# Kernel tuning notes

Measured on AMD Instinct MI355X. Metric: run time of the kernel, lower is better.

The kernel has to match this reference:

```python
import jax, jax.numpy as jnp
import numpy as np

LAMBDA_A = 1.0
NUM_ITER = 3
K = 64
BN_EPS = 1e-5


def setup_inputs() -> dict:
    key = jax.random.key(0)
    ks = jax.random.split(key, 8)
    B, C, H, W = 16, 512, 64, 64
    x = jax.random.normal(ks[0], (B, C, H, W), dtype=jnp.float32)
    # codebook mu: init normal(std~sqrt(2/k)) then L2-normalize along dim=1 (k axis), as in torch init
    mu = jax.random.normal(ks[1], (C, K), dtype=jnp.float32) * np.sqrt(2.0 / K)
    mu = mu / jnp.maximum(jnp.linalg.norm(mu, axis=1, keepdims=True), 1e-12)
    # 1x1 convs expressed as (out, in) matrices
    stem_w = jax.random.normal(ks[2], (C, C), dtype=jnp.float32) * np.sqrt(2.0 / C)
    stem_b = jnp.zeros((C,), dtype=jnp.float32)
    head_w = jax.random.normal(ks[3], (C, C), dtype=jnp.float32) * np.sqrt(2.0 / C)
    head_b = jnp.zeros((C,), dtype=jnp.float32)
    bn_gamma = jnp.ones((C,), dtype=jnp.float32)
    bn_beta = jnp.zeros((C,), dtype=jnp.float32)
    return {"x": x, "mu": mu, "stem_w": stem_w, "stem_b": stem_b,
            "head_w": head_w, "head_b": head_b,
            "bn_gamma": bn_gamma, "bn_beta": bn_beta}


def _conv1x1(x, w, b):
    # x: (B,C,H,W), w: (O,C)
    return jnp.einsum('bchw,oc->bohw', x, w) + b[None, :, None, None]


def reference(x, mu, stem_w, stem_b, head_w, head_b, bn_gamma, bn_beta):
    B, C, H, W = x.shape
    N = H * W
    y = _conv1x1(x, stem_w, stem_b)                 # (B,C,H,W)
    yf = y.reshape(B, C, N).transpose(0, 2, 1)      # (B,N,C)

    mu_b = jnp.broadcast_to(mu[None], (B, C, K))    # (B,C,K)
    z = None
    for _ in range(NUM_ITER):
        z = jax.nn.softmax(LAMBDA_A * jnp.einsum('bnc,bck->bnk', yf, mu_b), axis=2)
        zn = z / (1e-6 + z.sum(axis=1, keepdims=True))
        mu_b = jnp.einsum('bnc,bnk->bck', yf, zn)
        mu_b = mu_b / jnp.maximum(jnp.linalg.norm(mu_b, axis=1, keepdims=True), 1e-12)

    # EM loop runs under no_grad in torch
    mu_b = jax.lax.stop_gradient(mu_b)
    z = jax.lax.stop_gradient(z)

    y2 = jnp.einsum('bck,bnk->bcn', mu_b, z).reshape(B, C, H, W)

    # head: ReLU -> 1x1 conv -> BatchNorm2d (training-mode batch stats)
    h = _conv1x1(jnp.maximum(y2, 0.0), head_w, head_b)
    mean = h.mean(axis=(0, 2, 3), keepdims=True)
    var = h.var(axis=(0, 2, 3), keepdims=True)
    h = (h - mean) * jax.lax.rsqrt(var + BN_EPS)
    h = h * bn_gamma[None, :, None, None] + bn_beta[None, :, None, None]

    return jnp.maximum(h + x, 0.0)
```

## Files before the change

### kernel.cpp

```cpp
#include <hip/hip_runtime.h>


typedef _Float16 half_t;
typedef _Float16 half4 __attribute__((ext_vector_type(4)));
typedef _Float16 half8 __attribute__((ext_vector_type(8)));
typedef float f32x4 __attribute__((ext_vector_type(4)));

#define GLD_LDS(gp, lp) __builtin_amdgcn_global_load_lds( \
    (const __attribute__((address_space(1))) void*)(gp),  \
    (__attribute__((address_space(3))) void*)(lp), 16, 0, 0)

#define SBAR __builtin_amdgcn_sched_barrier(0)
#define RAWBAR do { SBAR; __builtin_amdgcn_s_barrier(); SBAR; } while (0)

template <int L> __device__ __forceinline__ void vmwait() {
  if constexpr (L == 8) asm volatile("s_waitcnt vmcnt(8)" ::: "memory");
  else if constexpr (L == 6) asm volatile("s_waitcnt vmcnt(6)" ::: "memory");
  else asm volatile("s_waitcnt vmcnt(0)" ::: "memory");
}

constexpr int CB = 16;
constexpr int CC = 512;
constexpr int CN = 4096;
constexpr int CKK = 64;
constexpr long MALL = (long)CB * CN;

__device__ inline int swz8(int bid, int n) {
  return (bid & 7) * (n >> 3) + (bid >> 3);
}

__global__ __launch_bounds__(256) void prep(
    const float* __restrict__ stem_w, const float* __restrict__ head_w,
    const float* __restrict__ mu,
    half_t* __restrict__ swh, half_t* __restrict__ hwh,
    half_t* __restrict__ muT, half_t* __restrict__ muck)
{
  int i = blockIdx.x * 256 + threadIdx.x;
  swh[i] = (half_t)stem_w[i];
  hwh[i] = (half_t)head_w[i];
  if (i < CC * CKK) {
    int c = i >> 6, k = i & 63;
    half_t v = (half_t)mu[i];
    for (int b = 0; b < CB; ++b) {
      muT[(long)b * CKK * CC + (long)k * CC + c] = v;
      muck[(long)b * CC * CKK + i] = v;
    }
  }
}

__global__ __launch_bounds__(256) void xpose(
    const float* __restrict__ in, half_t* __restrict__ outT)
{
  __shared__ half_t t[64][65];
  const int s0 = blockIdx.x * 64, r0 = blockIdx.y * 64;
  const long bz = blockIdx.z;
  const float* ib = in + bz * (long)CC * CN;
  half_t* ob = outT + bz * (long)CC * CN;
  const int tid = threadIdx.x, cl = tid & 63, rw = tid >> 6;
#pragma unroll
  for (int it = 0; it < 16; ++it) {
    int r = it * 4 + rw;
    t[cl][r] = (half_t)ib[(long)(r0 + r) * CN + s0 + cl];
  }
  __syncthreads();
#pragma unroll
  for (int it = 0; it < 16; ++it) {
    int s = it * 4 + rw;
    ob[(long)(s0 + s) * CC + r0 + cl] = t[s][cl];
  }
}

template <int BM, int BN, int MODE, int EPI, bool SWZ>
__global__ __launch_bounds__(256) void gemm_abt(
    const half_t* __restrict__ A, const half_t* __restrict__ Bm,
    half_t* __restrict__ Co, half_t* __restrict__ CoT,
    float* __restrict__ Cacc, const float* __restrict__ bias,
    int M, int Nn, int Kk, int ksplit, long sA, long sB, long sC)
{
  constexpr int FM = BM / 32, FN = BN / 32;
  constexpr int HB = (BM + BN) * 64;
  constexpr int LCNT = (BM / 8) / 4 + (BN / 8) / 4;
  constexpr int STG = 2 * HB;
  constexpr int EPS = (EPI != 0) ? BN * (BM + 4) : 0;
  constexpr int TOT = STG > EPS ? STG : EPS;
  __shared__ __align__(16) half_t smem[TOT];

  const int tid = threadIdx.x, wid = tid >> 6, lane = tid & 63;
  int bid = blockIdx.x;
  if constexpr (SWZ) bid = swz8(bid, gridDim.x);
  const int tilesN = Nn / BN;
  const int tm = bid / tilesN, tn = bid % tilesN;
  const long bz = blockIdx.z;
  const half_t* Ab = A + bz * sA + (long)tm * BM * Kk;
  const half_t* Bb = Bm + bz * sB + (long)tn * BN * Kk;
  const int ksteps = Kk >> 6;
  const int per = ksteps / ksplit;
  const int ks0 = blockIdx.y * per, ks1 = ks0 + per;
  const int wr = wid >> 1, wc = wid & 1;

  const int r8 = lane >> 3;
  const int gcs = ((lane & 7) ^ r8) * 8;

  auto stage = [&](int ks, int buf) {
    half_t* dA = smem + buf * HB;
    half_t* dB = dA + BM * 64;
    const half_t* ga = Ab + (long)ks * 64;
#pragma unroll
    for (int c = wid; c < BM / 8; c += 4)
      GLD_LDS(ga + (long)(c * 8 + r8) * Kk + gcs, &dA[c * 512]);
    const half_t* gb = Bb + (long)ks * 64;
#pragma unroll
    for (int c = wid; c < BN / 8; c += 4)
      GLD_LDS(gb + (long)(c * 8 + r8) * Kk + gcs, &dB[c * 512]);
  };

  f32x4 acc[FM][FN];
#pragma unroll
  for (int i = 0; i < FM; ++i)
#pragma unroll
    for (int j = 0; j < FN; ++j) acc[i][j] = f32x4{0.f, 0.f, 0.f, 0.f};

  stage(ks0, 0);
  if (ks0 + 1 < ks1) { stage(ks0 + 1, 1); vmwait<LCNT>(); }
  else               { vmwait<0>(); }
  RAWBAR;

  int cur = 0;
  for (int ks = ks0; ks < ks1; ++ks) {
    const half_t* lA = smem + cur * HB;
    const half_t* lB = lA + BM * 64;
#pragma unroll
    for (int kk = 0; kk < 2; ++kk) {
      half8 af[FM], bfr[FN];
      const int cg = kk * 4 + (lane >> 4);
#pragma unroll
      for (int i = 0; i < FM; ++i) {
        const int rA = wr * (BM / 2) + i * 16 + (lane & 15);
        af[i] = *(const half8*)&lA[rA * 64 + ((cg ^ (rA & 7)) << 3)];
      }
#pragma unroll
      for (int j = 0; j < FN; ++j) {
        const int rB = wc * (BN / 2) + j * 16 + (lane & 15);
        bfr[j] = *(const half8*)&lB[rB * 64 + ((cg ^ (rB & 7)) << 3)];
      }
      __builtin_amdgcn_s_setprio(1);
#pragma unroll
      for (int i = 0; i < FM; ++i)
#pragma unroll
        for (int j = 0; j < FN; ++j)
          acc[i][j] = __builtin_amdgcn_mfma_f32_16x16x32_f16(af[i], bfr[j],
                                                             acc[i][j], 0, 0, 0);
      __builtin_amdgcn_s_setprio(0);
    }
    RAWBAR;
    const bool more = (ks + 2 < ks1);
    if (more) { stage(ks + 2, cur); vmwait<LCNT>(); }
    else      { vmwait<0>(); }
    RAWBAR;
    cur ^= 1;
  }

  if constexpr (EPI != 0) {
    static_assert(BM == 128 && BN == 128, "LDS epilogue assumes 128x128");
    constexpr int PIT = BM + 4;
    half_t* ep = smem;
#pragma unroll
    for (int j = 0; j < FN; ++j) {
      const int nl = wc * 64 + j * 16 + (lane & 15);
      float bv = 0.f;
      if constexpr (MODE & 1) bv = bias[tn * BN + nl];
#pragma unroll
      for (int i = 0; i < FM; ++i) {
        const int ml = wr * 64 + i * 16 + ((lane >> 4) << 2);
        half4 h;
#pragma unroll
        for (int r = 0; r < 4; ++r) {
          float v = acc[i][j][r] + bv;
          if constexpr (MODE & 2) v = fmaxf(v, 0.f);
          h[r] = (half_t)v;
        }
        *(half4*)&ep[nl * PIT + ml] = h;
      }
    }
    __syncthreads();
    const long rowbase = (long)tm * BM;
    if constexpr (EPI & 1) {
#pragma unroll
      for (int s = 0; s < 8; ++s) {
        const int q = tid + 256 * s;
        const int m = q & 127, cc = q >> 7;
        half8 v;
#pragma unroll
        for (int e = 0; e < 8; ++e) v[e] = ep[(cc * 8 + e) * PIT + m];
        *(half8*)&Co[bz * sC + (rowbase + m) * Nn + tn * BN + cc * 8] = v;
      }
    }
    if constexpr (EPI & 2) {
      const long b = rowbase >> 12, nbase = rowbase & 4095;
#pragma unroll
      for (int s = 0; s < 8; ++s) {
        const int q = tid + 256 * s;
        const int mc = q & 15;
        const int cl = q >> 4;
        half8 v = *(const half8*)&ep[cl * PIT + mc * 8];
        *(half8*)&CoT[(b * Nn + tn * BN + cl) * 4096 + nbase + mc * 8] = v;
      }
    }
  } else {
#pragma unroll
    for (int j = 0; j < FN; ++j) {
      const int n = tn * BN + wc * (BN / 2) + j * 16 + (lane & 15);
      float bv = 0.f;
      if constexpr (MODE & 1) bv = bias[n];
#pragma unroll
      for (int i = 0; i < FM; ++i) {
        const int mbase = tm * BM + wr * (BM / 2) + i * 16 + ((lane >> 4) << 2);
#pragma unroll
        for (int r = 0; r < 4; ++r) {
          const long idx = bz * sC + (long)(mbase + r) * Nn + n;
          if constexpr ((MODE & 4) != 0) {
            atomicAdd(&Cacc[idx], acc[i][j][r]);
          } else {
            float v = acc[i][j][r] + bv;
            if constexpr ((MODE & 2) != 0) v = fmaxf(v, 0.f);
            Co[idx] = (half_t)v;
          }
        }
      }
    }
  }
}

__global__ __launch_bounds__(256) void s_softmax(
    const half_t* __restrict__ Yf, const half_t* __restrict__ muT,
    half_t* __restrict__ zp, half_t* __restrict__ zT)
{
  constexpr int HB = (128 + 64) * 64;
  __shared__ __align__(16) union {
    half_t st[2 * HB];
    half_t zh[128 * 68];
  } sm;
  const int tid = threadIdx.x, wid = tid >> 6, lane = tid & 63;
  const int tm = blockIdx.x;
  const long bz = blockIdx.z;
  const half_t* Ab = Yf + bz * (long)CN * CC + (long)tm * 128 * CC;
  const half_t* Bb = muT + bz * (long)CKK * CC;

  const int r8 = lane >> 3;
  const int gcs = ((lane & 7) ^ r8) * 8;

  auto stage = [&](int ks, int buf) {
    half_t* dA = sm.st + buf * HB;
    half_t* dB = dA + 128 * 64;
    const half_t* ga = Ab + (long)ks * 64;
#pragma unroll
    for (int c = wid; c < 16; c += 4)
      GLD_LDS(ga + (long)(c * 8 + r8) * CC + gcs, &dA[c * 512]);
    const half_t* gb = Bb + (long)ks * 64;
#pragma unroll
    for (int c = wid; c < 8; c += 4)
      GLD_LDS(gb + (long)(c * 8 + r8) * CC + gcs, &dB[c * 512]);
  };

  f32x4 acc[2][4];
#pragma unroll
  for (int i = 0; i < 2; ++i)
#pragma unroll
    for (int j = 0; j < 4; ++j) acc[i][j] = f32x4{0.f, 0.f, 0.f, 0.f};

  stage(0, 0);
  stage(1, 1);
  vmwait<6>();
  RAWBAR;
  int cur = 0;
  for (int ks = 0; ks < 8; ++ks) {
    const half_t* lA = sm.st + cur * HB;
    const half_t* lB = lA + 128 * 64;
#pragma unroll
    for (int kk = 0; kk < 2; ++kk) {
      half8 af[2], bfr[4];
      const int cg = kk * 4 + (lane >> 4);
#pragma unroll
      for (int i = 0; i < 2; ++i) {
        const int rA = wid * 32 + i * 16 + (lane & 15);
        af[i] = *(const half8*)&lA[rA * 64 + ((cg ^ (rA & 7)) << 3)];
      }
#pragma unroll
      for (int j = 0; j < 4; ++j) {
        const int rB = j * 16 + (lane & 15);
        bfr[j] = *(const half8*)&lB[rB * 64 + ((cg ^ (rB & 7)) << 3)];
      }
      __builtin_amdgcn_s_setprio(1);
#pragma unroll
      for (int i = 0; i < 2; ++i)
#pragma unroll
        for (int j = 0; j < 4; ++j)
          acc[i][j] = __builtin_amdgcn_mfma_f32_16x16x32_f16(af[i], bfr[j],
                                                             acc[i][j], 0, 0, 0);
      __builtin_amdgcn_s_setprio(0);
    }
    RAWBAR;
    const bool more = (ks + 2 < 8);
    if (more) { stage(ks + 2, cur); vmwait<6>(); }
    else      { vmwait<0>(); }
    RAWBAR;
    cur ^= 1;
  }

#pragma unroll
  for (int i = 0; i < 2; ++i)
#pragma unroll
    for (int r = 0; r < 4; ++r) {
      float mx = fmaxf(fmaxf(acc[i][0][r], acc[i][1][r]),
                       fmaxf(acc[i][2][r], acc[i][3][r]));
#pragma unroll
      for (int m = 1; m < 16; m <<= 1) mx = fmaxf(mx, __shfl_xor(mx, m));
      float p[4], s = 0.f;
#pragma unroll
      for (int j = 0; j < 4; ++j) { p[j] = __expf(acc[i][j][r] - mx); s += p[j]; }
#pragma unroll
      for (int m = 1; m < 16; m <<= 1) s += __shfl_xor(s, m);
      const float inv = 1.f / s;
#pragma unroll
      for (int j = 0; j < 4; ++j) acc[i][j][r] = p[j] * inv;
    }

#pragma unroll
  for (int i = 0; i < 2; ++i)
#pragma unroll
    for (int j = 0; j < 4; ++j)
#pragma unroll
      for (int r = 0; r < 4; ++r) {
        const int row = wid * 32 + i * 16 + ((lane >> 4) << 2) + r;
        const int col = j * 16 + (lane & 15);
        sm.zh[row * 68 + col] = (half_t)acc[i][j][r];
      }
  __syncthreads();
  if (zp) {
    const int nl = tid >> 1, seg = tid & 1;
    const long base = bz * (long)CN * CKK + (long)(tm * 128 + nl) * CKK + seg * 32;
#pragma unroll
    for (int g = 0; g < 4; ++g) {
      half8 v;
#pragma unroll
      for (int e = 0; e < 8; ++e) v[e] = sm.zh[nl * 68 + seg * 32 + g * 8 + e];
      *(half8*)&zp[base + g * 8] = v;
    }
  }
  {
    const int k = tid >> 2, seg = tid & 3;
    const long base = bz * (long)CKK * CN + (long)k * CN + tm * 128 + seg * 32;
#pragma unroll
    for (int g = 0; g < 4; ++g) {
      half8 v;
#pragma unroll
      for (int e = 0; e < 8; ++e) v[e] = sm.zh[(seg * 32 + g * 8 + e) * 68 + k];
      *(half8*)&zT[base + g * 8] = v;
    }
  }
}

__global__ __launch_bounds__(64) void mu_norm(
    const float* __restrict__ acc, half_t* __restrict__ muT, half_t* __restrict__ muck)
{
  const int bk = blockIdx.x;
  const int b = bk >> 6, k = bk & 63;
  const float* row = acc + (long)bk * CC;
  const int t = threadIdx.x;
  float v[8]; float s = 0.f;
#pragma unroll
  for (int e = 0; e < 8; ++e) { v[e] = row[t * 8 + e]; s += v[e] * v[e]; }
#pragma unroll
  for (int m = 1; m < 64; m <<= 1) s += __shfl_xor(s, m);
  const float inv = 1.f / fmaxf(sqrtf(s), 1e-12f);
  half8 o;
#pragma unroll
  for (int e = 0; e < 8; ++e) o[e] = (half_t)(v[e] * inv);
  *(half8*)&muT[(long)bk * CC + t * 8] = o;
  half_t* mc = muck + (long)b * CC * CKK;
#pragma unroll
  for (int e = 0; e < 8; ++e) mc[(long)(t * 8 + e) * CKK + k] = o[e];
}

__global__ __launch_bounds__(256) void bn_stats2(
    const half_t* __restrict__ hcn, float* __restrict__ stats)
{
  const int c = blockIdx.x, tid = threadIdx.x;
  float s = 0.f, s2 = 0.f;
  for (int b = 0; b < CB; ++b) {
    const half_t* p = hcn + ((long)b * CC + c) * CN;
    for (int i = tid * 8; i < CN; i += 2048) {
      half8 v = *(const half8*)&p[i];
#pragma unroll
      for (int e = 0; e < 8; ++e) { float f = (float)v[e]; s += f; s2 += f * f; }
    }
  }
#pragma unroll
  for (int m = 1; m < 64; m <<= 1) { s += __shfl_xor(s, m); s2 += __shfl_xor(s2, m); }
  __shared__ float r[8];
  const int wid = tid >> 6;
  if ((tid & 63) == 0) { r[wid] = s; r[4 + wid] = s2; }
  __syncthreads();
  if (tid == 0) {
    stats[c] = r[0] + r[1] + r[2] + r[3];
    stats[CC + c] = r[4] + r[5] + r[6] + r[7];
  }
}

__global__ void bn_param(const float* __restrict__ stats,
                         const float* __restrict__ gamma, const float* __restrict__ beta,
                         float* __restrict__ scsh)
{
  const int c = threadIdx.x;
  const float cnt = 1.f / 65536.f;
  const float mean = stats[c] * cnt;
  const float var = stats[CC + c] * cnt - mean * mean;
  const float sc = gamma[c] * rsqrtf(var + 1e-5f);
  scsh[c] = sc;
  scsh[CC + c] = beta[c] - mean * sc;
}

__global__ __launch_bounds__(256) void bn_final2(
    const half_t* __restrict__ hcn, const float* __restrict__ x,
    const float* __restrict__ scsh, float* __restrict__ out)
{
  const long i8 = (long)blockIdx.x * 256 + threadIdx.x;
  const int c = (int)((i8 >> 9) & 511);
  const float sc = scsh[c], sh = scsh[CC + c];
  half8 h = *(const half8*)&hcn[i8 * 8];
  f32x4 x0 = *(const f32x4*)&x[i8 * 8];
  f32x4 x1 = *(const f32x4*)&x[i8 * 8 + 4];
  f32x4 o0, o1;
#pragma unroll
  for (int e = 0; e < 4; ++e) o0[e] = fmaxf((float)h[e] * sc + sh + x0[e], 0.f);
#pragma unroll
  for (int e = 0; e < 4; ++e) o1[e] = fmaxf((float)h[4 + e] * sc + sh + x1[e], 0.f);
  *(f32x4*)&out[i8 * 8] = o0;
  *(f32x4*)&out[i8 * 8 + 4] = o1;
}

extern "C" void kernel_launch(void* const* d_in, const int* in_sizes, int n_in,
                              void* d_out, int out_size, void* d_ws, size_t ws_size,
                              hipStream_t stream)
{
  const float* x      = (const float*)d_in[0];
  const float* mu     = (const float*)d_in[1];
  const float* stem_w = (const float*)d_in[2];
  const float* stem_b = (const float*)d_in[3];
  const float* head_w = (const float*)d_in[4];
  const float* head_b = (const float*)d_in[5];
  const float* bn_g   = (const float*)d_in[6];
  const float* bn_b   = (const float*)d_in[7];
  float* out = (float*)d_out;

  const size_t NEED = 214ull << 20;
  if (ws_size < NEED) {
    hipMemsetAsync(d_out, 0, (size_t)out_size * 4, stream);
    return;
  }
  char* ws = (char*)d_ws;
  const long MB = 1 << 20;
  half_t* xT   = (half_t*)(ws);
  half_t* Yf   = (half_t*)(ws + 64 * MB);
  half_t* ycn  = (half_t*)(ws + 128 * MB);
  half_t* z    = (half_t*)(ws + 192 * MB);
  half_t* zT   = (half_t*)(ws + 200 * MB);
  half_t* muT  = (half_t*)(ws + 208 * MB);
  half_t* muck = (half_t*)(ws + 209 * MB);
  float* muacc = (float*)(ws + 210 * MB);
  half_t* swh  = (half_t*)(ws + 212 * MB);
  half_t* hwh  = (half_t*)(ws + 212 * MB + 512 * 1024);
  float* stats = (float*)(ws + 213 * MB);
  float* scsh  = (float*)(ws + 213 * MB + 8 * 1024);
  half_t* y2f = xT;
  half_t* hcn = Yf;

  prep<<<1024, 256, 0, stream>>>(stem_w, head_w, mu, swh, hwh, muT, muck);
  xpose<<<dim3(64, 8, 16), 256, 0, stream>>>(x, xT);
  gemm_abt<128, 128, 1, 3, true><<<dim3(2048, 1, 1), 256, 0, stream>>>(
      xT, swh, Yf, ycn, nullptr, stem_b, (int)MALL, CC, CC, 1, 0, 0, 0);

  for (int it = 0; it < 3; ++it) {
    s_softmax<<<dim3(32, 1, 16), 256, 0, stream>>>(
        Yf, muT, (it == 2) ? z : nullptr, zT);
    hipMemsetAsync(muacc, 0, (size_t)CB * CKK * CC * 4, stream);
    gemm_abt<64, 128, 4, 0, false><<<dim3(4, 4, 16), 256, 0, stream>>>(
        zT, ycn, nullptr, nullptr, muacc, nullptr, CKK, CC, CN, 4,
        (long)CKK * CN, (long)CC * CN, (long)CKK * CC);
    mu_norm<<<CB * CKK, 64, 0, stream>>>(muacc, muT, muck);
  }
  gemm_abt<128, 128, 2, 1, true><<<dim3(128, 1, 16), 256, 0, stream>>>(
      z, muck, y2f, nullptr, nullptr, nullptr, CN, CC, CKK, 1,
      (long)CN * CKK, (long)CC * CKK, (long)CN * CC);
  gemm_abt<128, 128, 1, 2, true><<<dim3(2048, 1, 1), 256, 0, stream>>>(
      y2f, hwh, nullptr, hcn, nullptr, head_b, (int)MALL, CC, CC, 1, 0, 0, 0);

  bn_stats2<<<CC, 256, 0, stream>>>(hcn, stats);
  bn_param<<<1, 512, 0, stream>>>(stats, bn_g, bn_b, scsh);
  bn_final2<<<16384, 256, 0, stream>>>(hcn, x, scsh, out);
}
```

Before: 411.6 us.

## Add A-resident full-width GEMM for 1x1 convs and fuse BN statistics into head epilogue

Adds a new GEMM kernel that keeps a 64-row A tile (all 512 input channels) in LDS and computes all 512 output channels per block, streaming double-buffered weight slices with XOR-swizzled LDS layouts. It replaces both the stem and head 1x1 convolutions, so each activation row is read once instead of once per output tile. The head GEMM epilogue now accumulates per-channel sum and sum of squares with atomics, which removes the separate bn_stats2 pass over hcn. The cost is one block per CU at 512 threads with large LDS use, plus float atomic contention on the stats buffer, which also makes those sums non-deterministic.

```diff
diff --git a/kernel.cpp b/kernel.cpp
--- a/kernel.cpp
+++ b/kernel.cpp
@@ -16,6 +16,7 @@
 template <int L> __device__ __forceinline__ void vmwait() {
   if constexpr (L == 8) asm volatile("s_waitcnt vmcnt(8)" ::: "memory");
   else if constexpr (L == 6) asm volatile("s_waitcnt vmcnt(6)" ::: "memory");
+  else if constexpr (L == 4) asm volatile("s_waitcnt vmcnt(4)" ::: "memory");
   else asm volatile("s_waitcnt vmcnt(0)" ::: "memory");
 }
 
@@ -67,6 +68,135 @@
   for (int it = 0; it < 16; ++it) {
     int s = it * 4 + rw;
     ob[(long)(s0 + s) * CC + r0 + cl] = t[s][cl];
+  }
+}
+
+template <int MODE, int EPI, bool STATS>
+__global__ __launch_bounds__(512, 1) void gemm_ares(
+    const half_t* __restrict__ A, const half_t* __restrict__ Bw,
+    const float* __restrict__ bias,
+    half_t* __restrict__ Co, half_t* __restrict__ CoT,
+    float* __restrict__ stats)
+{
+  __shared__ __align__(16) half_t lA[64 * 512];
+  __shared__ __align__(16) half_t lB[2][512 * 32];
+  const int tid = threadIdx.x, wid = tid >> 6, lane = tid & 63;
+  const int g = lane >> 4;
+  const long row0 = (long)blockIdx.x * 64;
+
+  {
+#pragma unroll
+    for (int q = 0; q < 8; ++q) {
+      const int r = q * 8 + wid;
+      const int schunk = lane ^ (r & 7);
+      GLD_LDS(A + (row0 + r) * 512 + schunk * 8, &lA[r * 512]);
+    }
+  }
+  auto stageB = [&](int s, int b) {
+#pragma unroll
+    for (int q = 0; q < 4; ++q) {
+      const int t = wid * 4 + q;
+      const int o = t * 16 + (lane >> 2);
+      const int cg = (lane & 3) ^ ((o >> 1) & 3);
+      GLD_LDS(Bw + (long)o * 512 + s * 32 + cg * 8, &lB[b][t * 512]);
+    }
+  };
+
+  f32x4 acc[4][4];
+#pragma unroll
+  for (int i = 0; i < 4; ++i)
+#pragma unroll
+    for (int j = 0; j < 4; ++j) acc[i][j] = f32x4{0.f, 0.f, 0.f, 0.f};
+
+  stageB(0, 0);
+  stageB(1, 1);
+  vmwait<4>();
+  RAWBAR;
+
+  for (int s = 0; s < 16; ++s) {
+    const half_t* bb = &lB[s & 1][0];
+    half8 af[4], bf[4];
+#pragma unroll
+    for (int i = 0; i < 4; ++i) {
+      const int mr = i * 16 + (lane & 15);
+      const int c8 = (s * 4 + g) ^ (mr & 7);
+      af[i] = *(const half8*)&lA[mr * 512 + c8 * 8];
+    }
+#pragma unroll
+    for (int j = 0; j < 4; ++j) {
+      const int orr = wid * 64 + j * 16 + (lane & 15);
+      const int cg = g ^ ((orr >> 1) & 3);
+      bf[j] = *(const half8*)&bb[orr * 32 + cg * 8];
+    }
+    __builtin_amdgcn_s_setprio(1);
+#pragma unroll
+    for (int i = 0; i < 4; ++i)
+#pragma unroll
+      for (int j = 0; j < 4; ++j)
+        acc[i][j] = __builtin_amdgcn_mfma_f32_16x16x32_f16(af[i], bf[j],
+                                                           acc[i][j], 0, 0, 0);
+    __builtin_amdgcn_s_setprio(0);
+    RAWBAR;
+    if (s + 2 < 16) { stageB(s + 2, s & 1); vmwait<4>(); }
+    else            { vmwait<0>(); }
+    RAWBAR;
+  }
+
+  half_t* ep = &lB[0][0];
+#pragma unroll
+  for (int j = 0; j < 4; ++j) {
+    const int o = wid * 64 + j * 16 + (lane & 15);
+    const float bv = bias[o];
+    float s1 = 0.f, s2 = 0.f;
+#pragma unroll
+    for (int i = 0; i < 4; ++i) {
+      const int mbase = i * 16 + g * 4;
+      half4 h;
+#pragma unroll
+      for (int r = 0; r < 4; ++r) {
+        float v = acc[i][j][r] + bv;
+        if constexpr (MODE & 2) v = fmaxf(v, 0.f);
+        if constexpr (STATS) { s1 += v; s2 += v * v; }
+        h[r] = (half_t)v;
+      }
+      const int mc = (mbase >> 3) ^ (o & 7);
+      *(half4*)&ep[o * 64 + mc * 8 + (mbase & 7)] = h;
+    }
+    if constexpr (STATS) {
+      s1 += __shfl_xor(s1, 16); s1 += __shfl_xor(s1, 32);
+      s2 += __shfl_xor(s2, 16); s2 += __shfl_xor(s2, 32);
+      if (lane < 16) {
+        atomicAdd(&stats[o], s1);
+        atomicAdd(&stats[CC + o], s2);
+      }
+    }
+  }
+  __syncthreads();
+  const long b = row0 >> 12, nbase = row0 & 4095;
+  if constexpr (EPI & 1) {
+#pragma unroll
+    for (int p = 0; p < 8; ++p) {
+      const int q = p * 512 + tid;
+      const int m = q >> 6, ch = q & 63;
+      half8 v;
+#pragma unroll
+      for (int e = 0; e < 8; ++e) {
+        const int o = ch * 8 + e;
+        const int mc = (m >> 3) ^ (o & 7);
+        v[e] = ep[o * 64 + mc * 8 + (m & 7)];
+      }
+      *(half8*)&Co[(row0 + m) * 512 + ch * 8] = v;
+    }
+  }
+  if constexpr (EPI & 2) {
+#pragma unroll
+    for (int p = 0; p < 8; ++p) {
+      const int q = p * 512 + tid;
+      const int o = q >> 3, mc = q & 7;
+      const int mcs = mc ^ (o & 7);
+      half8 v = *(const half8*)&ep[o * 64 + mcs * 8];
+      *(half8*)&CoT[(b * CC + o) * 4096 + nbase + mc * 8] = v;
+    }
   }
 }
 
@@ -195,17 +325,6 @@
         *(half8*)&Co[bz * sC + (rowbase + m) * Nn + tn * BN + cc * 8] = v;
       }
     }
-    if constexpr (EPI & 2) {
-      const long b = rowbase >> 12, nbase = rowbase & 4095;
-#pragma unroll
-      for (int s = 0; s < 8; ++s) {
-        const int q = tid + 256 * s;
-        const int mc = q & 15;
-        const int cl = q >> 4;
-        half8 v = *(const half8*)&ep[cl * PIT + mc * 8];
-        *(half8*)&CoT[(b * Nn + tn * BN + cl) * 4096 + nbase + mc * 8] = v;
-      }
-    }
   } else {
 #pragma unroll
     for (int j = 0; j < FN; ++j) {
@@ -380,31 +499,6 @@
   half_t* mc = muck + (long)b * CC * CKK;
 #pragma unroll
   for (int e = 0; e < 8; ++e) mc[(long)(t * 8 + e) * CKK + k] = o[e];
-}
-
-__global__ __launch_bounds__(256) void bn_stats2(
-    const half_t* __restrict__ hcn, float* __restrict__ stats)
-{
-  const int c = blockIdx.x, tid = threadIdx.x;
-  float s = 0.f, s2 = 0.f;
-  for (int b = 0; b < CB; ++b) {
-    const half_t* p = hcn + ((long)b * CC + c) * CN;
-    for (int i = tid * 8; i < CN; i += 2048) {
-      half8 v = *(const half8*)&p[i];
-#pragma unroll
-      for (int e = 0; e < 8; ++e) { float f = (float)v[e]; s += f; s2 += f * f; }
-    }
-  }
-#pragma unroll
-  for (int m = 1; m < 64; m <<= 1) { s += __shfl_xor(s, m); s2 += __shfl_xor(s2, m); }
-  __shared__ float r[8];
-  const int wid = tid >> 6;
-  if ((tid & 63) == 0) { r[wid] = s; r[4 + wid] = s2; }
-  __syncthreads();
-  if (tid == 0) {
-    stats[c] = r[0] + r[1] + r[2] + r[3];
-    stats[CC + c] = r[4] + r[5] + r[6] + r[7];
-  }
 }
 
 __global__ void bn_param(const float* __restrict__ stats,
@@ -477,8 +571,8 @@
 
   prep<<<1024, 256, 0, stream>>>(stem_w, head_w, mu, swh, hwh, muT, muck);
   xpose<<<dim3(64, 8, 16), 256, 0, stream>>>(x, xT);
-  gemm_abt<128, 128, 1, 3, true><<<dim3(2048, 1, 1), 256, 0, stream>>>(
-      xT, swh, Yf, ycn, nullptr, stem_b, (int)MALL, CC, CC, 1, 0, 0, 0);
+  gemm_ares<1, 3, false><<<1024, 512, 0, stream>>>(
+      xT, swh, stem_b, Yf, ycn, nullptr);
 
   for (int it = 0; it < 3; ++it) {
     s_softmax<<<dim3(32, 1, 16), 256, 0, stream>>>(
@@ -492,10 +586,10 @@
   gemm_abt<128, 128, 2, 1, true><<<dim3(128, 1, 16), 256, 0, stream>>>(
       z, muck, y2f, nullptr, nullptr, nullptr, CN, CC, CKK, 1,
       (long)CN * CKK, (long)CC * CKK, (long)CN * CC);
-  gemm_abt<128, 128, 1, 2, true><<<dim3(2048, 1, 1), 256, 0, stream>>>(
-      y2f, hwh, nullptr, hcn, nullptr, head_b, (int)MALL, CC, CC, 1, 0, 0, 0);
-
-  bn_stats2<<<CC, 256, 0, stream>>>(hcn, stats);
+  hipMemsetAsync(stats, 0, 2 * CC * sizeof(float), stream);
+  gemm_ares<1, 2, true><<<1024, 512, 0, stream>>>(
+      y2f, hwh, head_b, nullptr, hcn, stats);
+
   bn_param<<<1, 512, 0, stream>>>(stats, bn_g, bn_b, scsh);
   bn_final2<<<16384, 256, 0, stream>>>(hcn, x, scsh, out);
 }
```

Measured after the change: 493.2 us. 19.8% more time.

## Fuse fp32 transpose-convert of x into stem GEMM A-operand loading

Applied to the files above, without the earlier changes.

Removes the separate xpose kernel that converted x to fp16 and transposed it, and adds a dedicated stem GEMM that loads fp32 x directly with strided per-thread reads, converts it in registers and writes it swizzled into LDS. The weight tile still goes through async global-to-LDS loads. This drops a full write and read of a 64MB intermediate. In exchange, A loads are now 32 scalar fp32 loads per thread across rows that are synchronously waited before the LDS write, which weakens the load/compute overlap.

```diff
diff --git a/kernel.cpp b/kernel.cpp
--- a/kernel.cpp
+++ b/kernel.cpp
@@ -12,10 +12,12 @@
 
 #define SBAR __builtin_amdgcn_sched_barrier(0)
 #define RAWBAR do { SBAR; __builtin_amdgcn_s_barrier(); SBAR; } while (0)
+#define LGKM0 do { asm volatile("s_waitcnt lgkmcnt(0)" ::: "memory"); SBAR; } while (0)
 
 template <int L> __device__ __forceinline__ void vmwait() {
   if constexpr (L == 8) asm volatile("s_waitcnt vmcnt(8)" ::: "memory");
   else if constexpr (L == 6) asm volatile("s_waitcnt vmcnt(6)" ::: "memory");
+  else if constexpr (L == 4) asm volatile("s_waitcnt vmcnt(4)" ::: "memory");
   else asm volatile("s_waitcnt vmcnt(0)" ::: "memory");
 }
 
@@ -48,25 +50,141 @@
   }
 }
 
-__global__ __launch_bounds__(256) void xpose(
-    const float* __restrict__ in, half_t* __restrict__ outT)
-{
-  __shared__ half_t t[64][65];
-  const int s0 = blockIdx.x * 64, r0 = blockIdx.y * 64;
-  const long bz = blockIdx.z;
-  const float* ib = in + bz * (long)CC * CN;
-  half_t* ob = outT + bz * (long)CC * CN;
-  const int tid = threadIdx.x, cl = tid & 63, rw = tid >> 6;
-#pragma unroll
-  for (int it = 0; it < 16; ++it) {
-    int r = it * 4 + rw;
-    t[cl][r] = (half_t)ib[(long)(r0 + r) * CN + s0 + cl];
+template <bool SWZ>
+__global__ __launch_bounds__(256) void gemm_stem(
+    const float* __restrict__ X, const half_t* __restrict__ Bw,
+    const float* __restrict__ bias,
+    half_t* __restrict__ Co, half_t* __restrict__ CoT)
+{
+  constexpr int SAB = 16384;
+  __shared__ __align__(16) half_t smem[2 * SAB];
+  const int tid = threadIdx.x, wid = tid >> 6, lane = tid & 63;
+  int bid = blockIdx.x;
+  if constexpr (SWZ) bid = swz8(bid, gridDim.x);
+  const int tm = bid >> 2, tn = bid & 3;
+  const long row0 = (long)tm * 128;
+  const long b = row0 >> 12;
+  const int n0 = (int)(row0 & 4095);
+  const float* Xb = X + b * ((long)CC * CN) + n0;
+  const half_t* Bb = Bw + (long)tn * 128 * CC;
+  const int wr = wid >> 1, wc = wid & 1;
+
+  const int an = tid & 127;
+  const int ac0 = (tid >> 7) * 32;
+  const int r8 = lane >> 3;
+  const int gcs = ((lane & 7) ^ r8) * 8;
+
+  float va[32];
+  auto issueA = [&](int ks) {
+    const float* p = Xb + (long)(ks * 64 + ac0) * CN + an;
+#pragma unroll
+    for (int e = 0; e < 32; ++e) va[e] = p[(long)e * CN];
+  };
+  auto writeA = [&](int buf) {
+    half_t* dA = smem + buf * SAB;
+#pragma unroll
+    for (int g = 0; g < 4; ++g) {
+      half8 h;
+#pragma unroll
+      for (int e = 0; e < 8; ++e) h[e] = (half_t)va[g * 8 + e];
+      const int chunk = (ac0 >> 3) + g;
+      *(half8*)&dA[an * 64 + ((chunk ^ (an & 7)) << 3)] = h;
+    }
+  };
+  auto stageB = [&](int ks, int buf) {
+    half_t* dB = smem + buf * SAB + 8192;
+    const half_t* gb = Bb + (long)ks * 64;
+#pragma unroll
+    for (int c = wid; c < 16; c += 4)
+      GLD_LDS(gb + (long)(c * 8 + r8) * CC + gcs, &dB[c * 512]);
+  };
+
+  f32x4 acc[4][4];
+#pragma unroll
+  for (int i = 0; i < 4; ++i)
+#pragma unroll
+    for (int j = 0; j < 4; ++j) acc[i][j] = f32x4{0.f, 0.f, 0.f, 0.f};
+
+  issueA(0);
+  stageB(0, 0);
+  vmwait<0>();
+  writeA(0);
+  LGKM0;
+  RAWBAR;
+
+  int cur = 0;
+  for (int ks = 0; ks < 8; ++ks) {
+    if (ks < 7) { issueA(ks + 1); stageB(ks + 1, cur ^ 1); }
+    const half_t* lA = smem + cur * SAB;
+    const half_t* lB = lA + 8192;
+#pragma unroll
+    for (int kk = 0; kk < 2; ++kk) {
+      half8 af[4], bfr[4];
+      const int cg = kk * 4 + (lane >> 4);
+#pragma unroll
+      for (int i = 0; i < 4; ++i) {
+        const int rA = wr * 64 + i * 16 + (lane & 15);
+        af[i] = *(const half8*)&lA[rA * 64 + ((cg ^ (rA & 7)) << 3)];
+      }
+#pragma unroll
+      for (int j = 0; j < 4; ++j) {
+        const int rB = wc * 64 + j * 16 + (lane & 15);
+        bfr[j] = *(const half8*)&lB[rB * 64 + ((cg ^ (rB & 7)) << 3)];
+      }
+      __builtin_amdgcn_s_setprio(1);
+#pragma unroll
+      for (int i = 0; i < 4; ++i)
+#pragma unroll
+        for (int j = 0; j < 4; ++j)
+          acc[i][j] = __builtin_amdgcn_mfma_f32_16x16x32_f16(af[i], bfr[j],
+                                                             acc[i][j], 0, 0, 0);
+      __builtin_amdgcn_s_setprio(0);
+    }
+    RAWBAR;
+    if (ks < 7) {
+      vmwait<0>();
+      writeA(cur ^ 1);
+      LGKM0;
+    }
+    RAWBAR;
+    cur ^= 1;
+  }
+
+  constexpr int PIT = 132;
+  half_t* ep = smem;
+#pragma unroll
+  for (int j = 0; j < 4; ++j) {
+    const int nl = wc * 64 + j * 16 + (lane & 15);
+    const float bv = bias[tn * 128 + nl];
+#pragma unroll
+    for (int i = 0; i < 4; ++i) {
+      const int ml = wr * 64 + i * 16 + ((lane >> 4) << 2);
+      half4 h;
+#pragma unroll
+      for (int r = 0; r < 4; ++r) h[r] = (half_t)(acc[i][j][r] + bv);
+      *(half4*)&ep[nl * PIT + ml] = h;
+    }
   }
   __syncthreads();
-#pragma unroll
-  for (int it = 0; it < 16; ++it) {
-    int s = it * 4 + rw;
-    ob[(long)(s0 + s) * CC + r0 + cl] = t[s][cl];
+  {
+#pragma unroll
+    for (int s = 0; s < 8; ++s) {
+      const int q = tid + 256 * s;
+      const int m = q & 127, cc8 = q >> 7;
+      half8 v;
+#pragma unroll
+      for (int e = 0; e < 8; ++e) v[e] = ep[(cc8 * 8 + e) * PIT + m];
+      *(half8*)&Co[(row0 + m) * CC + tn * 128 + cc8 * 8] = v;
+    }
+  }
+  {
+#pragma unroll
+    for (int s = 0; s < 8; ++s) {
+      const int q = tid + 256 * s;
+      const int mc = q & 15, cl = q >> 4;
+      half8 v = *(const half8*)&ep[cl * PIT + mc * 8];
+      *(half8*)&CoT[(b * CC + tn * 128 + cl) * CN + n0 + mc * 8] = v;
+    }
   }
 }
 
@@ -188,11 +306,11 @@
 #pragma unroll
       for (int s = 0; s < 8; ++s) {
         const int q = tid + 256 * s;
-        const int m = q & 127, cc = q >> 7;
+        const int m = q & 127, cc8 = q >> 7;
         half8 v;
 #pragma unroll
-        for (int e = 0; e < 8; ++e) v[e] = ep[(cc * 8 + e) * PIT + m];
-        *(half8*)&Co[bz * sC + (rowbase + m) * Nn + tn * BN + cc * 8] = v;
+        for (int e = 0; e < 8; ++e) v[e] = ep[(cc8 * 8 + e) * PIT + m];
+        *(half8*)&Co[bz * sC + (rowbase + m) * Nn + tn * BN + cc8 * 8] = v;
       }
     }
     if constexpr (EPI & 2) {
@@ -200,8 +318,7 @@
 #pragma unroll
       for (int s = 0; s < 8; ++s) {
         const int q = tid + 256 * s;
-        const int mc = q & 15;
-        const int cl = q >> 4;
+        const int mc = q & 15, cl = q >> 4;
         half8 v = *(const half8*)&ep[cl * PIT + mc * 8];
         *(half8*)&CoT[(b * Nn + tn * BN + cl) * 4096 + nbase + mc * 8] = v;
       }
@@ -460,7 +577,7 @@
   }
   char* ws = (char*)d_ws;
   const long MB = 1 << 20;
-  half_t* xT   = (half_t*)(ws);
+  half_t* y2f  = (half_t*)(ws);
   half_t* Yf   = (half_t*)(ws + 64 * MB);
   half_t* ycn  = (half_t*)(ws + 128 * MB);
   half_t* z    = (half_t*)(ws + 192 * MB);
@@ -472,13 +589,10 @@
   half_t* hwh  = (half_t*)(ws + 212 * MB + 512 * 1024);
   float* stats = (float*)(ws + 213 * MB);
   float* scsh  = (float*)(ws + 213 * MB + 8 * 1024);
-  half_t* y2f = xT;
   half_t* hcn = Yf;
 
   prep<<<1024, 256, 0, stream>>>(stem_w, head_w, mu, swh, hwh, muT, muck);
-  xpose<<<dim3(64, 8, 16), 256, 0, stream>>>(x, xT);
-  gemm_abt<128, 128, 1, 3, true><<<dim3(2048, 1, 1), 256, 0, stream>>>(
-      xT, swh, Yf, ycn, nullptr, stem_b, (int)MALL, CC, CC, 1, 0, 0, 0);
+  gemm_stem<true><<<2048, 256, 0, stream>>>(x, swh, stem_b, Yf, ycn);
 
   for (int it = 0; it < 3; ++it) {
     s_softmax<<<dim3(32, 1, 16), 256, 0, stream>>>(
```

Measured after the change: 400.6 us. 1.03x faster.

## Fuse BN statistics into head GEMM epilogue and single-buffer GEMM staging

Applied to the files above, without the earlier changes.

Removes the separate bn_stats2 pass. Per-channel sum and sum-of-squares are now accumulated in the head GEMM epilogue with wave shuffles and float atomics, which avoids re-reading the head output. Both GEMM kernels also drop double-buffered LDS prefetch in favour of a single buffer with a full vmcnt(0) wait each k-step. This shrinks LDS use and may raise occupancy, but load latency is no longer overlapped with compute. The mu-update GEMM's k-split goes from 4 to 8, and stats are computed from fp32 values before the fp16 rounding of the stored output.

```diff
diff --git a/kernel.cpp b/kernel.cpp
--- a/kernel.cpp
+++ b/kernel.cpp
@@ -12,12 +12,7 @@
 
 #define SBAR __builtin_amdgcn_sched_barrier(0)
 #define RAWBAR do { SBAR; __builtin_amdgcn_s_barrier(); SBAR; } while (0)
-
-template <int L> __device__ __forceinline__ void vmwait() {
-  if constexpr (L == 8) asm volatile("s_waitcnt vmcnt(8)" ::: "memory");
-  else if constexpr (L == 6) asm volatile("s_waitcnt vmcnt(6)" ::: "memory");
-  else asm volatile("s_waitcnt vmcnt(0)" ::: "memory");
-}
+#define VM0   do { asm volatile("s_waitcnt vmcnt(0)" ::: "memory"); SBAR; } while (0)
 
 constexpr int CB = 16;
 constexpr int CC = 512;
@@ -70,19 +65,18 @@
   }
 }
 
-template <int BM, int BN, int MODE, int EPI, bool SWZ>
+template <int BM, int BN, int MODE, int EPI, bool SWZ, bool STATS>
 __global__ __launch_bounds__(256) void gemm_abt(
     const half_t* __restrict__ A, const half_t* __restrict__ Bm,
     half_t* __restrict__ Co, half_t* __restrict__ CoT,
     float* __restrict__ Cacc, const float* __restrict__ bias,
+    float* __restrict__ stats,
     int M, int Nn, int Kk, int ksplit, long sA, long sB, long sC)
 {
   constexpr int FM = BM / 32, FN = BN / 32;
   constexpr int HB = (BM + BN) * 64;
-  constexpr int LCNT = (BM / 8) / 4 + (BN / 8) / 4;
-  constexpr int STG = 2 * HB;
   constexpr int EPS = (EPI != 0) ? BN * (BM + 4) : 0;
-  constexpr int TOT = STG > EPS ? STG : EPS;
+  constexpr int TOT = HB > EPS ? HB : EPS;
   __shared__ __align__(16) half_t smem[TOT];
 
   const int tid = threadIdx.x, wid = tid >> 6, lane = tid & 63;
@@ -101,9 +95,9 @@
   const int r8 = lane >> 3;
   const int gcs = ((lane & 7) ^ r8) * 8;
 
-  auto stage = [&](int ks, int buf) {
-    half_t* dA = smem + buf * HB;
-    half_t* dB = dA + BM * 64;
+  auto stage = [&](int ks) {
+    half_t* dA = smem;
+    half_t* dB = smem + BM * 64;
     const half_t* ga = Ab + (long)ks * 64;
 #pragma unroll
     for (int c = wid; c < BM / 8; c += 4)
@@ -120,15 +114,12 @@
 #pragma unroll
     for (int j = 0; j < FN; ++j) acc[i][j] = f32x4{0.f, 0.f, 0.f, 0.f};
 
-  stage(ks0, 0);
-  if (ks0 + 1 < ks1) { stage(ks0 + 1, 1); vmwait<LCNT>(); }
-  else               { vmwait<0>(); }
-  RAWBAR;
-
-  int cur = 0;
   for (int ks = ks0; ks < ks1; ++ks) {
-    const half_t* lA = smem + cur * HB;
-    const half_t* lB = lA + BM * 64;
+    stage(ks);
+    VM0;
+    RAWBAR;
+    const half_t* lA = smem;
+    const half_t* lB = smem + BM * 64;
 #pragma unroll
     for (int kk = 0; kk < 2; ++kk) {
       half8 af[FM], bfr[FN];
@@ -153,11 +144,6 @@
       __builtin_amdgcn_s_setprio(0);
     }
     RAWBAR;
-    const bool more = (ks + 2 < ks1);
-    if (more) { stage(ks + 2, cur); vmwait<LCNT>(); }
-    else      { vmwait<0>(); }
-    RAWBAR;
-    cur ^= 1;
   }
 
   if constexpr (EPI != 0) {
@@ -169,6 +155,7 @@
       const int nl = wc * 64 + j * 16 + (lane & 15);
       float bv = 0.f;
       if constexpr (MODE & 1) bv = bias[tn * BN + nl];
+      float s1 = 0.f, s2 = 0.f;
 #pragma unroll
       for (int i = 0; i < FM; ++i) {
         const int ml = wr * 64 + i * 16 + ((lane >> 4) << 2);
@@ -177,10 +164,20 @@
         for (int r = 0; r < 4; ++r) {
           float v = acc[i][j][r] + bv;
           if constexpr (MODE & 2) v = fmaxf(v, 0.f);
+          if constexpr (STATS) { s1 += v; s2 += v * v; }
           h[r] = (half_t)v;
         }
         *(half4*)&ep[nl * PIT + ml] = h;
       }
+      if constexpr (STATS) {
+        s1 += __shfl_xor(s1, 16); s1 += __shfl_xor(s1, 32);
+        s2 += __shfl_xor(s2, 16); s2 += __shfl_xor(s2, 32);
+        if (lane < 16) {
+          const int ch = tn * BN + nl;
+          atomicAdd(&stats[ch], s1);
+          atomicAdd(&stats[CC + ch], s2);
+        }
+      }
     }
     __syncthreads();
     const long rowbase = (long)tm * BM;
@@ -188,11 +185,11 @@
 #pragma unroll
       for (int s = 0; s < 8; ++s) {
         const int q = tid + 256 * s;
-        const int m = q & 127, cc = q >> 7;
+        const int m = q & 127, cc8 = q >> 7;
         half8 v;
 #pragma unroll
-        for (int e = 0; e < 8; ++e) v[e] = ep[(cc * 8 + e) * PIT + m];
-        *(half8*)&Co[bz * sC + (rowbase + m) * Nn + tn * BN + cc * 8] = v;
+        for (int e = 0; e < 8; ++e) v[e] = ep[(cc8 * 8 + e) * PIT + m];
+        *(half8*)&Co[bz * sC + (rowbase + m) * Nn + tn * BN + cc8 * 8] = v;
       }
     }
     if constexpr (EPI & 2) {
@@ -200,8 +197,7 @@
 #pragma unroll
       for (int s = 0; s < 8; ++s) {
         const int q = tid + 256 * s;
-        const int mc = q & 15;
-        const int cl = q >> 4;
+        const int mc = q & 15, cl = q >> 4;
         half8 v = *(const half8*)&ep[cl * PIT + mc * 8];
         *(half8*)&CoT[(b * Nn + tn * BN + cl) * 4096 + nbase + mc * 8] = v;
       }
@@ -237,7 +233,7 @@
 {
   constexpr int HB = (128 + 64) * 64;
   __shared__ __align__(16) union {
-    half_t st[2 * HB];
+    half_t st[HB];
     half_t zh[128 * 68];
   } sm;
   const int tid = threadIdx.x, wid = tid >> 6, lane = tid & 63;
@@ -249,9 +245,9 @@
   const int r8 = lane >> 3;
   const int gcs = ((lane & 7) ^ r8) * 8;
 
-  auto stage = [&](int ks, int buf) {
-    half_t* dA = sm.st + buf * HB;
-    half_t* dB = dA + 128 * 64;
+  auto stage = [&](int ks) {
+    half_t* dA = sm.st;
+    half_t* dB = sm.st + 128 * 64;
     const half_t* ga = Ab + (long)ks * 64;
 #pragma unroll
     for (int c = wid; c < 16; c += 4)
@@ -268,14 +264,12 @@
 #pragma unroll
     for (int j = 0; j < 4; ++j) acc[i][j] = f32x4{0.f, 0.f, 0.f, 0.f};
 
-  stage(0, 0);
-  stage(1, 1);
-  vmwait<6>();
-  RAWBAR;
-  int cur = 0;
   for (int ks = 0; ks < 8; ++ks) {
-    const half_t* lA = sm.st + cur * HB;
-    const half_t* lB = lA + 128 * 64;
+    stage(ks);
+    VM0;
+    RAWBAR;
+    const half_t* lA = sm.st;
+    const half_t* lB = sm.st + 128 * 64;
 #pragma unroll
     for (int kk = 0; kk < 2; ++kk) {
       half8 af[2], bfr[4];
@@ -300,11 +294,6 @@
       __builtin_amdgcn_s_setprio(0);
     }
     RAWBAR;
-    const bool more = (ks + 2 < 8);
-    if (more) { stage(ks + 2, cur); vmwait<6>(); }
-    else      { vmwait<0>(); }
-    RAWBAR;
-    cur ^= 1;
   }
 
 #pragma unroll
@@ -380,31 +369,6 @@
   half_t* mc = muck + (long)b * CC * CKK;
 #pragma unroll
   for (int e = 0; e < 8; ++e) mc[(long)(t * 8 + e) * CKK + k] = o[e];
-}
-
-__global__ __launch_bounds__(256) void bn_stats2(
-    const half_t* __restrict__ hcn, float* __restrict__ stats)
-{
-  const int c = blockIdx.x, tid = threadIdx.x;
-  float s = 0.f, s2 = 0.f;
-  for (int b = 0; b < CB; ++b) {
-    const half_t* p = hcn + ((long)b * CC + c) * CN;
-    for (int i = tid * 8; i < CN; i += 2048) {
-      half8 v = *(const half8*)&p[i];
-#pragma unroll
-      for (int e = 0; e < 8; ++e) { float f = (float)v[e]; s += f; s2 += f * f; }
-    }
-  }
-#pragma unroll
-  for (int m = 1; m < 64; m <<= 1) { s += __shfl_xor(s, m); s2 += __shfl_xor(s2, m); }
-  __shared__ float r[8];
-  const int wid = tid >> 6;
-  if ((tid & 63) == 0) { r[wid] = s; r[4 + wid] = s2; }
-  __syncthreads();
-  if (tid == 0) {
-    stats[c] = r[0] + r[1] + r[2] + r[3];
-    stats[CC + c] = r[4] + r[5] + r[6] + r[7];
-  }
 }
 
 __global__ void bn_param(const float* __restrict__ stats,
@@ -477,25 +441,25 @@
 
   prep<<<1024, 256, 0, stream>>>(stem_w, head_w, mu, swh, hwh, muT, muck);
   xpose<<<dim3(64, 8, 16), 256, 0, stream>>>(x, xT);
-  gemm_abt<128, 128, 1, 3, true><<<dim3(2048, 1, 1), 256, 0, stream>>>(
-      xT, swh, Yf, ycn, nullptr, stem_b, (int)MALL, CC, CC, 1, 0, 0, 0);
+  gemm_abt<128, 128, 1, 3, true, false><<<dim3(2048, 1, 1), 256, 0, stream>>>(
+      xT, swh, Yf, ycn, nullptr, stem_b, nullptr, (int)MALL, CC, CC, 1, 0, 0, 0);
 
   for (int it = 0; it < 3; ++it) {
     s_softmax<<<dim3(32, 1, 16), 256, 0, stream>>>(
         Yf, muT, (it == 2) ? z : nullptr, zT);
     hipMemsetAsync(muacc, 0, (size_t)CB * CKK * CC * 4, stream);
-    gemm_abt<64, 128, 4, 0, false><<<dim3(4, 4, 16), 256, 0, stream>>>(
-        zT, ycn, nullptr, nullptr, muacc, nullptr, CKK, CC, CN, 4,
+    gemm_abt<64, 128, 4, 0, false, false><<<dim3(4, 8, 16), 256, 0, stream>>>(
+        zT, ycn, nullptr, nullptr, muacc, nullptr, nullptr, CKK, CC, CN, 8,
         (long)CKK * CN, (long)CC * CN, (long)CKK * CC);
     mu_norm<<<CB * CKK, 64, 0, stream>>>(muacc, muT, muck);
   }
-  gemm_abt<128, 128, 2, 1, true><<<dim3(128, 1, 16), 256, 0, stream>>>(
-      z, muck, y2f, nullptr, nullptr, nullptr, CN, CC, CKK, 1,
+  gemm_abt<128, 128, 2, 1, true, false><<<dim3(128, 1, 16), 256, 0, stream>>>(
+      z, muck, y2f, nullptr, nullptr, nullptr, nullptr, CN, CC, CKK, 1,
       (long)CN * CKK, (long)CC * CKK, (long)CN * CC);
-  gemm_abt<128, 128, 1, 2, true><<<dim3(2048, 1, 1), 256, 0, stream>>>(
-      y2f, hwh, nullptr, hcn, nullptr, head_b, (int)MALL, CC, CC, 1, 0, 0, 0);
-
-  bn_stats2<<<CC, 256, 0, stream>>>(hcn, stats);
+  hipMemsetAsync(stats, 0, 2 * CC * sizeof(float), stream);
+  gemm_abt<128, 128, 1, 2, true, true><<<dim3(2048, 1, 1), 256, 0, stream>>>(
+      y2f, hwh, nullptr, hcn, nullptr, head_b, stats, (int)MALL, CC, CC, 1, 0, 0, 0);
+
   bn_param<<<1, 512, 0, stream>>>(stats, bn_g, bn_b, scsh);
   bn_final2<<<16384, 256, 0, stream>>>(hcn, x, scsh, out);
 }
```

Measured after the change: 421.1 us. 1.02x slower.
